# Performance work log

Measured on AMD Instinct MI355X. Metric: run time of the kernel, lower is better.

The kernel has to match this reference:

```python
import jax, jax.numpy as jnp
import numpy as np

B, C, RXD, E, P, OSIZE = 64, 4, 64, 512, 4, 256


def setup_inputs() -> dict:
    key = jax.random.key(0)
    ks = jax.random.split(key, 6)
    x = jax.random.normal(ks[0], (B, C, RXD, E), dtype=jnp.float32)
    # rxd permutation (gather form of the one-hot permuteRxdMatrix matmul)
    rxd_perm = jax.random.permutation(ks[1], RXD)
    # E permutation and its compositions: permuter = permuter @ permuteEMatrix
    # in column-index form: idx_{p+1}[j] = idx_p[e_perm[j]]
    e_perm = np.array(jax.random.permutation(ks[2], E))
    idx = e_perm.copy()
    cols = []
    for _ in range(P):
        cols.append(idx.copy())
        idx = idx[e_perm]
    e_idx = jnp.asarray(np.stack(cols, axis=1))  # (E, P) int
    # sign selected at the single nonzero entry of each permutation column
    signs = (jax.random.uniform(ks[3], (E, P)) > 0.5).astype(jnp.float32) * 2.0 - 1.0
    fan_in = RXD * E * P
    W = jax.random.normal(ks[4], (OSIZE, fan_in), dtype=jnp.float32) / np.float32(np.sqrt(fan_in))
    b = jax.random.normal(ks[5], (OSIZE,), dtype=jnp.float32) * 0.01
    return {"x": x, "rxd_perm": rxd_perm, "e_idx": e_idx, "signs": signs, "W": W, "b": b}


def reference(x, rxd_perm, e_idx, signs, W, b):
    Bb, Cc, R, Ee = x.shape
    Pp = e_idx.shape[1]
    # permute rxd axis (exact equivalent of x.transpose @ one-hot matrix)
    out = x[:, :, rxd_perm, :]                      # (B,C,R,E)
    # signed E-permutations for all P powers (exact equiv of dense matmul
    # with permuteETensor * signTensor, which has one signed nonzero per column)
    out = out[..., e_idx] * signs                   # (B,C,R,E,P)
    L = R * Ee
    pieces = []
    for p in range(Pp):
        k = 2 ** p
        v = out[..., p].reshape(Bb, Cc, L)
        if k == 1:
            pieces.append(v)                        # pool+unpool with k=1 is identity
        else:
            Lp = ((L + k - 1) // k) * k             # ceil_mode padding
            vp = jnp.pad(v, ((0, 0), (0, 0), (0, Lp - L)), constant_values=-jnp.inf)
            w = vp.reshape(Bb, Cc, Lp // k, k)
            am = jnp.argmax(w, axis=-1)             # first max, matching torch MaxPool1d
            mx = jnp.max(w, axis=-1)
            onehot = jnp.arange(k) == am[..., None]
            # MaxUnpool: max value at argmax position, zeros elsewhere
            pieces.append(jnp.where(onehot, mx[..., None], 0.0).reshape(Bb, Cc, Lp))
    pieces[-1] = pieces[-1][:, :, :L]               # truncate last piece to L
    cat = jnp.concatenate(pieces, axis=2)           # (B,C,L*P) since L % k == 0
    return cat @ W.T + b                            # (B,C,OSIZE)
```

## Files before the change

### kernel.cpp

```cpp
#include <hip/hip_runtime.h>
#include <stdint.h>

#define B_ 64
#define C_ 4
#define R_ 64
#define E_ 512
#define P_ 4
#define OS_ 256
#define L_ 32768
#define K_ 131072
#define M_ 256

#define BM 256
#define BN 128
#define BK 32
#define Z_ 256
#define KCH (K_/Z_)
#define ITERS (KCH/BK)

#define XSTR 513

typedef float  floatx4 __attribute__((ext_vector_type(4)));
typedef short  shortx8 __attribute__((ext_vector_type(8)));

#define GLDS16(g, l) __builtin_amdgcn_global_load_lds(                      \
    (const __attribute__((address_space(1))) void*)(g),                     \
    (__attribute__((address_space(3))) void*)(l), 16, 0, 0)

static __device__ __forceinline__ unsigned short f2bf(float f) {
  union { float f; unsigned int u; } v; v.f = f;
  unsigned int u = v.u;
  u += 0x7fffu + ((u >> 16) & 1u);
  return (unsigned short)(u >> 16);
}

__global__ __launch_bounds__(512) void convW_k(
    const float* __restrict__ W, unsigned short* __restrict__ W2) {
  __shared__ __align__(16) unsigned short T[64 * 64 * 8];
  const int t    = threadIdx.x;
  const int lane = t & 63;
  const int wv   = t >> 6;
  const int kb   = blockIdx.x >> 1;
  const int nh   = blockIdx.x & 1;

  #pragma unroll 1
  for (int nt = 0; nt < 2; ++nt) {
    const int n0 = nh * 128 + nt * 64;
    #pragma unroll
    for (int j = 0; j < 8; ++j) {
      const int n = j * 8 + wv;
      const float* wp = W + (size_t)(n0 + n) * K_ + (size_t)kb * 512 + lane * 8;
      const float4 a0 = *(const float4*)(wp);
      const float4 a1 = *(const float4*)(wp + 4);
      shortx8 g;
      g[0] = (short)f2bf(a0.x); g[1] = (short)f2bf(a0.y);
      g[2] = (short)f2bf(a0.z); g[3] = (short)f2bf(a0.w);
      g[4] = (short)f2bf(a1.x); g[5] = (short)f2bf(a1.y);
      g[6] = (short)f2bf(a1.z); g[7] = (short)f2bf(a1.w);
      *(shortx8*)(&T[((size_t)lane * 64 + (n ^ lane)) * 8]) = g;
    }
    __syncthreads();
    #pragma unroll
    for (int i = 0; i < 8; ++i) {
      const int k8loc = wv * 8 + i;
      const shortx8 g = *(const shortx8*)(&T[((size_t)k8loc * 64 + (lane ^ k8loc)) * 8]);
      *(shortx8*)(W2 + ((size_t)(kb * 64 + k8loc) * 256 + n0 + lane) * 8) = g;
    }
    __syncthreads();
  }
}

__global__ __launch_bounds__(512) void build_A(
    const float* __restrict__ x, const int* __restrict__ rxd_perm,
    const int* __restrict__ e_idx, const float* __restrict__ signs,
    unsigned short* __restrict__ A2) {
  __shared__ __align__(16) float xr[32 * XSTR];
  const int t    = threadIdx.x;
  const int lane = t & 63;
  const int wv   = t >> 6;

  const int blk = blockIdx.x;
  const int r   = blk >> 3;
  const int bcg = blk & 7;
  const int pr  = rxd_perm[r];

  #pragma unroll
  for (int i = 0; i < 2; ++i) {
    const int row = wv * 4 + i * 2 + (lane >> 5);
    const float* xsrc = x + ((size_t)(bcg * 32 + row) * R_ + pr) * E_;
    float* xd = xr + (size_t)row * XSTR;
    #pragma unroll
    for (int pass = 0; pass < 8; ++pass) {
      const int e = pass * 64 + (lane & 31) * 2;
      const float2 v = *(const float2*)(xsrc + e);
      xd[e]     = v.x;
      xd[e + 1] = v.y;
    }
  }
  __syncthreads();

  const int bcl = t & 31;
  const int bc  = bcg * 32 + bcl;
  const float* xp = xr + (size_t)bcl * XSTR;

  #pragma unroll 1
  for (int task = 0; task < 4; ++task) {
    const int l  = task * 16 + (t >> 5);
    const int e0 = l * 8;

    float v[4][8];
    #pragma unroll
    for (int i = 0; i < 8; ++i) {
      const uint4  ei = *(const uint4*)(e_idx + (size_t)(e0 + i) * 4);
      const float4 sg = *(const float4*)(signs + (size_t)(e0 + i) * 4);
      v[0][i] = xp[ei.x] * sg.x;
      v[1][i] = xp[ei.y] * sg.y;
      v[2][i] = xp[ei.z] * sg.z;
      v[3][i] = xp[ei.w] * sg.w;
    }

    unsigned short* dst = A2 + ((size_t)(r * 64 + l) * 256 + bc) * 8;
    shortx8 o;

    #pragma unroll
    for (int i = 0; i < 8; ++i) o[i] = (short)f2bf(v[0][i]);
    *(shortx8*)(dst) = o;

    #pragma unroll
    for (int j = 0; j < 4; ++j) {
      const float a = v[1][2 * j], b = v[1][2 * j + 1];
      const bool first = (a >= b);
      o[2 * j]     = (short)f2bf(first ? a : 0.0f);
      o[2 * j + 1] = (short)f2bf(first ? 0.0f : b);
    }
    *(shortx8*)(dst + (size_t)4096 * 256 * 8) = o;

    #pragma unroll
    for (int j = 0; j < 2; ++j) {
      int am = 0; float m = v[2][4 * j];
      #pragma unroll
      for (int i = 1; i < 4; ++i)
        if (v[2][4 * j + i] > m) { m = v[2][4 * j + i]; am = i; }
      #pragma unroll
      for (int i = 0; i < 4; ++i) o[4 * j + i] = (short)f2bf(i == am ? m : 0.0f);
    }
    *(shortx8*)(dst + (size_t)2 * 4096 * 256 * 8) = o;

    {
      int am = 0; float m = v[3][0];
      #pragma unroll
      for (int i = 1; i < 8; ++i)
        if (v[3][i] > m) { m = v[3][i]; am = i; }
      #pragma unroll
      for (int i = 0; i < 8; ++i) o[i] = (short)f2bf(i == am ? m : 0.0f);
    }
    *(shortx8*)(dst + (size_t)3 * 4096 * 256 * 8) = o;
  }
}

__global__ __launch_bounds__(512, 4) void gemm_splitk(
    const unsigned short* __restrict__ A2, const unsigned short* __restrict__ W2,
    float* __restrict__ Pp) {
  __shared__ unsigned short As[2][4 * 256 * 8];
  __shared__ unsigned short Ws[2][4 * 128 * 8];
  const int t    = threadIdx.x;
  const int lane = t & 63;
  const int wv   = t >> 6;

  const int id = blockIdx.x;
  const int ny = (id >> 3) & 1;
  const int z  = (id & 7) | ((id >> 4) << 3);
  const int nBase = ny * BN;

  const int wm   = (wv >> 1) * 64;
  const int wn   = (wv & 1) * 64;
  const int lrow = lane & 15;
  const int quad = lane >> 4;

  floatx4 acc[4][4];
  #pragma unroll
  for (int i = 0; i < 4; ++i)
    #pragma unroll
    for (int j = 0; j < 4; ++j) acc[i][j] = {0.f, 0.f, 0.f, 0.f};

  auto stage = [&](int buf, int it) {
    const size_t g0 = (size_t)(z * 64 + it * 4) * 256;
    #pragma unroll
    for (int c = 0; c < 2; ++c) {
      const int slot = (wv * 2 + c) * 64 + lane;
      GLDS16(A2 + (g0 + slot) * 8, &As[buf][slot * 8]);
    }
    const int wslot = wv * 64 + lane;
    const int slab  = wslot >> 7;
    const int nloc  = wslot & 127;
    GLDS16(W2 + (g0 + (size_t)slab * 256 + nBase + nloc) * 8, &Ws[buf][wslot * 8]);
  };
  auto compute = [&](int buf) {
    shortx8 af[4], wf[4];
    #pragma unroll
    for (int ti = 0; ti < 4; ++ti)
      af[ti] = *(const shortx8*)(&As[buf][(quad * 256 + wm + ti * 16 + lrow) * 8]);
    #pragma unroll
    for (int tj = 0; tj < 4; ++tj)
      wf[tj] = *(const shortx8*)(&Ws[buf][(quad * 128 + wn + tj * 16 + lrow) * 8]);
    #pragma unroll
    for (int ti = 0; ti < 4; ++ti)
      #pragma unroll
      for (int tj = 0; tj < 4; ++tj)
        acc[ti][tj] = __builtin_amdgcn_mfma_f32_16x16x32_bf16(
            af[ti], wf[tj], acc[ti][tj], 0, 0, 0);
  };

  stage(0, 0);
  __syncthreads();

  for (int it = 0; it < ITERS; ++it) {
    const int b = it & 1;
    if (it + 1 < ITERS) stage(b ^ 1, it + 1);
    compute(b);
    __syncthreads();
  }

  float* Pz = Pp + (size_t)z * (M_ * OS_);
  #pragma unroll
  for (int ti = 0; ti < 4; ++ti)
    #pragma unroll
    for (int tj = 0; tj < 4; ++tj)
      #pragma unroll
      for (int j = 0; j < 4; ++j) {
        const int m = wm + ti * 16 + quad * 4 + j;
        const int n = nBase + wn + tj * 16 + lrow;
        Pz[(size_t)m * OS_ + n] = acc[ti][tj][j];
      }
}

__global__ __launch_bounds__(256) void reduce_out(
    const float* __restrict__ Pp, const float* __restrict__ bias,
    float* __restrict__ out) {
  __shared__ float4 part[128];
  const int t    = threadIdx.x;
  const int i4   = blockIdx.x * 128 + (t & 127);
  const int half = t >> 7;
  const float* p = Pp + (size_t)i4 * 4 + (size_t)half * 128 * (M_ * OS_);
  float4 s = {0.f, 0.f, 0.f, 0.f};
  #pragma unroll 8
  for (int zz = 0; zz < 128; ++zz) {
    const float4 v = *(const float4*)(p + (size_t)zz * (M_ * OS_));
    s.x += v.x; s.y += v.y; s.z += v.z; s.w += v.w;
  }
  if (half) part[t & 127] = s;
  __syncthreads();
  if (!half) {
    const float4 q = part[t];
    const float4 bb = *(const float4*)(bias + ((i4 * 4) & (OS_ - 1)));
    float4 o = {s.x + q.x + bb.x, s.y + q.y + bb.y,
                s.z + q.z + bb.z, s.w + q.w + bb.w};
    *(float4*)(out + (size_t)i4 * 4) = o;
  }
}

extern "C" void kernel_launch(void* const* d_in, const int* in_sizes, int n_in,
                              void* d_out, int out_size, void* d_ws, size_t ws_size,
                              hipStream_t stream) {
  const float* x        = (const float*)d_in[0];
  const int*   rxd_perm = (const int*)d_in[1];
  const int*   e_idx    = (const int*)d_in[2];
  const float* signs    = (const float*)d_in[3];
  const float* W        = (const float*)d_in[4];
  const float* bias     = (const float*)d_in[5];
  float* out = (float*)d_out;

  unsigned short* A2 = (unsigned short*)d_ws;
  unsigned short* W2 = (unsigned short*)((char*)d_ws + 67108864);
  float*          Pp = (float*)((char*)d_ws + 134217728);

  convW_k<<<dim3(512), dim3(512), 0, stream>>>(W, W2);
  build_A<<<dim3(512), dim3(512), 0, stream>>>(x, rxd_perm, e_idx, signs, A2);
  gemm_splitk<<<dim3(2 * Z_), dim3(512), 0, stream>>>(A2, W2, Pp);
  reduce_out<<<dim3(128), dim3(256), 0, stream>>>(Pp, bias, out);
}
```

Before: 302.7 us.

## Fuse W bf16 conversion into split-K GEMM, reading A fragments directly from global

Removes the separate convW kernel and its 64MB bf16 W2 round trip. Each GEMM block now loads its fp32 W slice, converts it to bf16 into a swizzled LDS tile, and streams A fragments straight from global memory into registers instead of double-buffering them through LDS. The grid grows to 1024 blocks, each owning a 64-column N tile, so A is read four times across the N tiles instead of twice. There is also no overlap of A global loads with the MFMA work.

```diff
diff --git a/kernel.cpp b/kernel.cpp
--- a/kernel.cpp
+++ b/kernel.cpp
@@ -12,62 +12,20 @@
 #define M_ 256
 
 #define BM 256
-#define BN 128
-#define BK 32
+#define BN 64
 #define Z_ 256
 #define KCH (K_/Z_)
-#define ITERS (KCH/BK)
 
 #define XSTR 513
 
 typedef float  floatx4 __attribute__((ext_vector_type(4)));
 typedef short  shortx8 __attribute__((ext_vector_type(8)));
-
-#define GLDS16(g, l) __builtin_amdgcn_global_load_lds(                      \
-    (const __attribute__((address_space(1))) void*)(g),                     \
-    (__attribute__((address_space(3))) void*)(l), 16, 0, 0)
 
 static __device__ __forceinline__ unsigned short f2bf(float f) {
   union { float f; unsigned int u; } v; v.f = f;
   unsigned int u = v.u;
   u += 0x7fffu + ((u >> 16) & 1u);
   return (unsigned short)(u >> 16);
-}
-
-__global__ __launch_bounds__(512) void convW_k(
-    const float* __restrict__ W, unsigned short* __restrict__ W2) {
-  __shared__ __align__(16) unsigned short T[64 * 64 * 8];
-  const int t    = threadIdx.x;
-  const int lane = t & 63;
-  const int wv   = t >> 6;
-  const int kb   = blockIdx.x >> 1;
-  const int nh   = blockIdx.x & 1;
-
-  #pragma unroll 1
-  for (int nt = 0; nt < 2; ++nt) {
-    const int n0 = nh * 128 + nt * 64;
-    #pragma unroll
-    for (int j = 0; j < 8; ++j) {
-      const int n = j * 8 + wv;
-      const float* wp = W + (size_t)(n0 + n) * K_ + (size_t)kb * 512 + lane * 8;
-      const float4 a0 = *(const float4*)(wp);
-      const float4 a1 = *(const float4*)(wp + 4);
-      shortx8 g;
-      g[0] = (short)f2bf(a0.x); g[1] = (short)f2bf(a0.y);
-      g[2] = (short)f2bf(a0.z); g[3] = (short)f2bf(a0.w);
-      g[4] = (short)f2bf(a1.x); g[5] = (short)f2bf(a1.y);
-      g[6] = (short)f2bf(a1.z); g[7] = (short)f2bf(a1.w);
-      *(shortx8*)(&T[((size_t)lane * 64 + (n ^ lane)) * 8]) = g;
-    }
-    __syncthreads();
-    #pragma unroll
-    for (int i = 0; i < 8; ++i) {
-      const int k8loc = wv * 8 + i;
-      const shortx8 g = *(const shortx8*)(&T[((size_t)k8loc * 64 + (lane ^ k8loc)) * 8]);
-      *(shortx8*)(W2 + ((size_t)(kb * 64 + k8loc) * 256 + n0 + lane) * 8) = g;
-    }
-    __syncthreads();
-  }
 }
 
 __global__ __launch_bounds__(512) void build_A(
@@ -158,78 +116,72 @@
   }
 }
 
-__global__ __launch_bounds__(512, 4) void gemm_splitk(
-    const unsigned short* __restrict__ A2, const unsigned short* __restrict__ W2,
+__global__ __launch_bounds__(512, 4) void gemm_fw(
+    const unsigned short* __restrict__ A2, const float* __restrict__ W,
     float* __restrict__ Pp) {
-  __shared__ unsigned short As[2][4 * 256 * 8];
-  __shared__ unsigned short Ws[2][4 * 128 * 8];
+  __shared__ unsigned short Ws[64 * 64 * 8];
   const int t    = threadIdx.x;
   const int lane = t & 63;
   const int wv   = t >> 6;
-
-  const int id = blockIdx.x;
-  const int ny = (id >> 3) & 1;
-  const int z  = (id & 7) | ((id >> 4) << 3);
-  const int nBase = ny * BN;
-
-  const int wm   = (wv >> 1) * 64;
-  const int wn   = (wv & 1) * 64;
+  const int id   = blockIdx.x;
+  const int z    = id & 255;
+  const int ny   = id >> 8;
   const int lrow = lane & 15;
   const int quad = lane >> 4;
 
-  floatx4 acc[4][4];
-  #pragma unroll
-  for (int i = 0; i < 4; ++i)
+  const float* wb = W + (size_t)(ny * 64) * K_ + (size_t)z * 512 + lane * 8;
+  float4 wa[8][2];
+  #pragma unroll
+  for (int i = 0; i < 8; ++i) {
+    const float* wp = wb + (size_t)(wv * 8 + i) * K_;
+    wa[i][0] = *(const float4*)(wp);
+    wa[i][1] = *(const float4*)(wp + 4);
+  }
+  #pragma unroll
+  for (int i = 0; i < 8; ++i) {
+    shortx8 g;
+    g[0] = (short)f2bf(wa[i][0].x); g[1] = (short)f2bf(wa[i][0].y);
+    g[2] = (short)f2bf(wa[i][0].z); g[3] = (short)f2bf(wa[i][0].w);
+    g[4] = (short)f2bf(wa[i][1].x); g[5] = (short)f2bf(wa[i][1].y);
+    g[6] = (short)f2bf(wa[i][1].z); g[7] = (short)f2bf(wa[i][1].w);
+    *(shortx8*)(&Ws[((size_t)lane * 64 + ((wv * 8 + i) ^ lane)) * 8]) = g;
+  }
+  __syncthreads();
+
+  floatx4 acc[2][4];
+  #pragma unroll
+  for (int i = 0; i < 2; ++i)
     #pragma unroll
     for (int j = 0; j < 4; ++j) acc[i][j] = {0.f, 0.f, 0.f, 0.f};
 
-  auto stage = [&](int buf, int it) {
-    const size_t g0 = (size_t)(z * 64 + it * 4) * 256;
-    #pragma unroll
-    for (int c = 0; c < 2; ++c) {
-      const int slot = (wv * 2 + c) * 64 + lane;
-      GLDS16(A2 + (g0 + slot) * 8, &As[buf][slot * 8]);
-    }
-    const int wslot = wv * 64 + lane;
-    const int slab  = wslot >> 7;
-    const int nloc  = wslot & 127;
-    GLDS16(W2 + (g0 + (size_t)slab * 256 + nBase + nloc) * 8, &Ws[buf][wslot * 8]);
-  };
-  auto compute = [&](int buf) {
-    shortx8 af[4], wf[4];
-    #pragma unroll
-    for (int ti = 0; ti < 4; ++ti)
-      af[ti] = *(const shortx8*)(&As[buf][(quad * 256 + wm + ti * 16 + lrow) * 8]);
+  const unsigned short* ab =
+      A2 + ((size_t)(z * 64 + quad) * 256 + wv * 32 + lrow) * 8;
+
+  #pragma unroll
+  for (int s = 0; s < 16; ++s) {
+    const shortx8 af0 = *(const shortx8*)(ab + (size_t)s * 8192);
+    const shortx8 af1 = *(const shortx8*)(ab + (size_t)s * 8192 + 128);
+    const int k8l = s * 4 + quad;
+    shortx8 wf[4];
     #pragma unroll
     for (int tj = 0; tj < 4; ++tj)
-      wf[tj] = *(const shortx8*)(&Ws[buf][(quad * 128 + wn + tj * 16 + lrow) * 8]);
-    #pragma unroll
-    for (int ti = 0; ti < 4; ++ti)
-      #pragma unroll
-      for (int tj = 0; tj < 4; ++tj)
-        acc[ti][tj] = __builtin_amdgcn_mfma_f32_16x16x32_bf16(
-            af[ti], wf[tj], acc[ti][tj], 0, 0, 0);
-  };
-
-  stage(0, 0);
-  __syncthreads();
-
-  for (int it = 0; it < ITERS; ++it) {
-    const int b = it & 1;
-    if (it + 1 < ITERS) stage(b ^ 1, it + 1);
-    compute(b);
-    __syncthreads();
-  }
-
-  float* Pz = Pp + (size_t)z * (M_ * OS_);
-  #pragma unroll
-  for (int ti = 0; ti < 4; ++ti)
+      wf[tj] = *(const shortx8*)(&Ws[((size_t)k8l * 64 + ((tj * 16 + lrow) ^ k8l)) * 8]);
+    #pragma unroll
+    for (int tj = 0; tj < 4; ++tj) {
+      acc[0][tj] = __builtin_amdgcn_mfma_f32_16x16x32_bf16(af0, wf[tj], acc[0][tj], 0, 0, 0);
+      acc[1][tj] = __builtin_amdgcn_mfma_f32_16x16x32_bf16(af1, wf[tj], acc[1][tj], 0, 0, 0);
+    }
+  }
+
+  float* Pz = Pp + (size_t)z * (M_ * OS_) + ny * 64;
+  #pragma unroll
+  for (int ti = 0; ti < 2; ++ti)
     #pragma unroll
     for (int tj = 0; tj < 4; ++tj)
       #pragma unroll
       for (int j = 0; j < 4; ++j) {
-        const int m = wm + ti * 16 + quad * 4 + j;
-        const int n = nBase + wn + tj * 16 + lrow;
+        const int m = wv * 32 + ti * 16 + quad * 4 + j;
+        const int n = tj * 16 + lrow;
         Pz[(size_t)m * OS_ + n] = acc[ti][tj][j];
       }
 }
@@ -271,11 +223,9 @@
   float* out = (float*)d_out;
 
   unsigned short* A2 = (unsigned short*)d_ws;
-  unsigned short* W2 = (unsigned short*)((char*)d_ws + 67108864);
-  float*          Pp = (float*)((char*)d_ws + 134217728);
-
-  convW_k<<<dim3(512), dim3(512), 0, stream>>>(W, W2);
+  float*          Pp = (float*)((char*)d_ws + 67108864);
+
   build_A<<<dim3(512), dim3(512), 0, stream>>>(x, rxd_perm, e_idx, signs, A2);
-  gemm_splitk<<<dim3(2 * Z_), dim3(512), 0, stream>>>(A2, W2, Pp);
+  gemm_fw<<<dim3(1024), dim3(512), 0, stream>>>(A2, W, Pp);
   reduce_out<<<dim3(128), dim3(256), 0, stream>>>(Pp, bias, out);
 }
```

Measured after the change: 275.6 us. -8.9%, faster.
